# Kernel optimization log

Measured on AMD Instinct MI355X. Metric: run time of the kernel, lower is better.

The kernel has to match this reference:

```python
import jax, jax.numpy as jnp
import numpy as np

N = 100000   # nodes
E = 800000   # edges
D = 128      # hidden_dim (= in_dim here)
H = 4        # heads
C = D // H   # per-head channels = 32
L = 3        # gat layers


def setup_inputs() -> dict:
    key = jax.random.key(0)
    ks = jax.random.split(key, 14)
    s = 0.05
    return {
        "x": jax.random.normal(ks[0], (N, D), dtype=jnp.float32),
        "edge_index": jax.random.randint(ks[1], (2, E), 0, N, dtype=jnp.int32),
        "w_in": jax.random.normal(ks[2], (D, D), dtype=jnp.float32) * s,
        "b_in": jnp.zeros((D,), jnp.float32),
        "Wl": jax.random.normal(ks[3], (L, D, D), dtype=jnp.float32) * s,   # lin_l weights
        "bl": jnp.zeros((L, D), jnp.float32),                               # lin_l bias
        "Wr": jax.random.normal(ks[4], (L, D, D), dtype=jnp.float32) * s,   # lin_r (no bias)
        "att": jax.random.normal(ks[5], (L, H, C), dtype=jnp.float32) * s,  # attention vector a
        "b_out": jnp.zeros((L, D), jnp.float32),                            # conv output bias
        "Wres": jax.random.normal(ks[6], (L - 1, D, D), dtype=jnp.float32) * s,  # residual projs i>0
        "bres": jnp.zeros((L - 1, D), jnp.float32),
        "ln_g": jnp.ones((L, D), jnp.float32),
        "ln_b": jnp.zeros((L, D), jnp.float32),
    }


def _layer_norm(x, g, b, eps=1e-5):
    mu = x.mean(-1, keepdims=True)
    var = ((x - mu) ** 2).mean(-1, keepdims=True)
    return (x - mu) * jax.lax.rsqrt(var + eps) * g + b


def _pairnorm(x, scale=1.0):
    xc = x - x.mean(0, keepdims=True)
    l2 = jnp.sqrt((xc * xc).sum(1, keepdims=True)) + 1e-6
    return xc / l2 * scale * jnp.sqrt(jnp.float32(x.shape[0]))


def _gatv2(x, src, dst, Wl, bl, Wr, att, b_out):
    # lin_l / lin_r projections -> [N, H, C]
    xl = (x @ Wl + bl).reshape(N, H, C)
    xr = (x @ Wr).reshape(N, H, C)
    # edge-wise message: leaky_relu(x_l[j] + x_r[i])  [E, H, C]
    m = jax.nn.leaky_relu(xl[src] + xr[dst], negative_slope=0.2)
    logits = (m * att).sum(-1)  # [E, H]
    # segment softmax over edges grouped by destination node
    lmax = jax.ops.segment_max(logits, dst, num_segments=N)  # [N, H]
    a = jnp.exp(logits - lmax[dst])
    denom = jax.ops.segment_sum(a, dst, num_segments=N)
    a = a / (denom[dst] + 1e-16)
    # aggregate alpha * x_l[j] into destinations, concat heads
    out = jax.ops.segment_sum(a[:, :, None] * xl[src], dst, num_segments=N)
    return out.reshape(N, D) + b_out


def reference(x, edge_index, w_in, b_in, Wl, bl, Wr, att, b_out, Wres, bres, ln_g, ln_b):
    src, dst = edge_index[0], edge_index[1]
    h = x @ w_in + b_in
    for i in range(L):
        identity = h if i == 0 else h @ Wres[i - 1] + bres[i - 1]
        h = _gatv2(h, src, dst, Wl[i], bl[i], Wr[i], att[i], b_out[i])
        h = _pairnorm(h)
        # dropout is identity in eval mode
        h = h + identity
        h = _layer_norm(h, ln_g[i], ln_b[i])
        if i < L - 1:
            h = jax.nn.relu(h)
    return h
```

## Files before the change

### kernel.cpp

```cpp
#include <hip/hip_runtime.h>
#include <hip/hip_bf16.h>

#define NN 100000
#define NE 800000

typedef __attribute__((ext_vector_type(8))) short bf16x8;
typedef __attribute__((ext_vector_type(4))) float f32x4;
typedef unsigned short ushort_t;

static __device__ __forceinline__ short f2bf(float f) {
    union { float f; unsigned u; } v; v.f = f;
    unsigned u = v.u;
    unsigned r = u + 0x7FFFu + ((u >> 16) & 1u);
    return (short)(r >> 16);
}
static __device__ __forceinline__ float bf2f(unsigned short u) {
    union { unsigned u; float f; } v; v.u = ((unsigned)u) << 16;
    return v.f;
}

__global__ void prep_w_k(const float* __restrict__ w_in, const float* __restrict__ Wl,
                         const float* __restrict__ Wr, const float* __restrict__ Wres,
                         ushort_t* __restrict__ wt)
{
    __shared__ float tile[32][33];
    int m = blockIdx.z;
    const float* src;
    if (m == 0)      src = w_in;
    else if (m < 4)  src = Wl + (size_t)(m - 1) * 16384;
    else if (m < 7)  src = Wr + (size_t)(m - 4) * 16384;
    else             src = Wres + (size_t)(m - 7) * 16384;
    ushort_t* dst = wt + (size_t)m * 16384;

    int tx = threadIdx.x, ty = threadIdx.y;
    int k0 = blockIdx.x * 32, c0 = blockIdx.y * 32;
    #pragma unroll
    for (int j = 0; j < 4; ++j)
        tile[ty + 8 * j][tx] = src[(size_t)(k0 + ty + 8 * j) * 128 + c0 + tx];
    __syncthreads();
    #pragma unroll
    for (int j = 0; j < 4; ++j)
        dst[(size_t)(c0 + ty + 8 * j) * 128 + k0 + tx] = (ushort_t)f2bf(tile[tx][ty + 8 * j]);
}

template<int A_FP32>
__global__ __launch_bounds__(256, 4)
void gemm_k(const void* __restrict__ Av, const ushort_t* __restrict__ wt,
            int w0, int w1, int w2,
            const float* __restrict__ bias0, const float* __restrict__ bias2,
            ushort_t* __restrict__ out0, int Dout0, ushort_t* __restrict__ out2, int M)
{
    __shared__ short Bs[128][136];
    const int tid = threadIdx.x;
    const int rowBlk = blockIdx.x * 128;
    const int y = blockIdx.y;
    const ushort_t* W = wt + (size_t)((y == 0) ? w0 : (y == 1) ? w1 : w2) * 16384;
    const float* bias = (y == 0) ? bias0 : ((y == 2) ? bias2 : nullptr);
    ushort_t* out = (y == 2) ? out2 : out0;
    const int Dout   = (y == 2) ? 128 : Dout0;
    const int colOff = (y == 1) ? 128 : 0;

    const int wave = tid >> 6;
    const int lane = tid & 63;
    const int quad = lane >> 4;
    const int lr   = lane & 15;

    const int row0 = rowBlk + wave * 32 + lr;
    const int row1 = row0 + 16;

    bf16x8 afr[4][2];
    #pragma unroll
    for (int ks = 0; ks < 4; ++ks) {
        int kb = ks * 32 + quad * 8;
        bf16x8 a0 = (bf16x8)0, a1 = (bf16x8)0;
        if (A_FP32) {
            const float* A = (const float*)Av;
            if (row0 < M) {
                float4 v0 = *(const float4*)(A + (size_t)row0 * 128 + kb);
                float4 v1 = *(const float4*)(A + (size_t)row0 * 128 + kb + 4);
                a0[0]=f2bf(v0.x); a0[1]=f2bf(v0.y); a0[2]=f2bf(v0.z); a0[3]=f2bf(v0.w);
                a0[4]=f2bf(v1.x); a0[5]=f2bf(v1.y); a0[6]=f2bf(v1.z); a0[7]=f2bf(v1.w);
            }
            if (row1 < M) {
                float4 v0 = *(const float4*)(A + (size_t)row1 * 128 + kb);
                float4 v1 = *(const float4*)(A + (size_t)row1 * 128 + kb + 4);
                a1[0]=f2bf(v0.x); a1[1]=f2bf(v0.y); a1[2]=f2bf(v0.z); a1[3]=f2bf(v0.w);
                a1[4]=f2bf(v1.x); a1[5]=f2bf(v1.y); a1[6]=f2bf(v1.z); a1[7]=f2bf(v1.w);
            }
        } else {
            const ushort_t* A = (const ushort_t*)Av;
            if (row0 < M) a0 = *(const bf16x8*)(A + (size_t)row0 * 128 + kb);
            if (row1 < M) a1 = *(const bf16x8*)(A + (size_t)row1 * 128 + kb);
        }
        afr[ks][0] = a0; afr[ks][1] = a1;
    }

    #pragma unroll
    for (int i = 0; i < 8; ++i) {
        int linear = tid + 256 * i;
        int r  = linear >> 4;
        int c8 = (linear & 15) << 3;
        *(bf16x8*)&Bs[r][c8] = *(const bf16x8*)(W + (size_t)r * 128 + c8);
    }
    __syncthreads();

    f32x4 acc[2][8];
    #pragma unroll
    for (int mt = 0; mt < 2; ++mt)
        #pragma unroll
        for (int nt = 0; nt < 8; ++nt) acc[mt][nt] = (f32x4)(0.0f);

    #pragma unroll
    for (int ks = 0; ks < 4; ++ks) {
        int kb = ks * 32 + quad * 8;
        #pragma unroll
        for (int nt = 0; nt < 8; ++nt) {
            bf16x8 b = *(const bf16x8*)&Bs[nt * 16 + lr][kb];
            acc[0][nt] = __builtin_amdgcn_mfma_f32_16x16x32_bf16(afr[ks][0], b, acc[0][nt], 0, 0, 0);
            acc[1][nt] = __builtin_amdgcn_mfma_f32_16x16x32_bf16(afr[ks][1], b, acc[1][nt], 0, 0, 0);
        }
    }

    __syncthreads();
    #pragma unroll
    for (int mt = 0; mt < 2; ++mt)
        #pragma unroll
        for (int nt = 0; nt < 8; ++nt) {
            int col = nt * 16 + lr;
            float b = bias ? bias[col] : 0.0f;
            #pragma unroll
            for (int r = 0; r < 4; ++r) {
                int row = wave * 32 + mt * 16 + quad * 4 + r;
                Bs[row][col] = f2bf(acc[mt][nt][r] + b);
            }
        }
    __syncthreads();
    #pragma unroll
    for (int i = 0; i < 8; ++i) {
        int linear = tid + 256 * i;
        int r  = linear >> 4;
        int c8 = (linear & 15) << 3;
        int gr = rowBlk + r;
        if (gr < M)
            *(bf16x8*)(out + (size_t)gr * Dout + colOff + c8) = *(const bf16x8*)&Bs[r][c8];
    }
}

__global__ void count_k(const int* __restrict__ dst, int* __restrict__ deg) {
    int e = blockIdx.x * 256 + threadIdx.x;
    if (e < NE) atomicAdd(&deg[dst[e]], 1);
}

__global__ void scan1_k(const int* __restrict__ deg, int* __restrict__ excl,
                        int* __restrict__ bsum) {
    __shared__ int buf[256];
    int i = blockIdx.x * 256 + threadIdx.x;
    int v = (i < NN) ? deg[i] : 0;
    buf[threadIdx.x] = v; __syncthreads();
    for (int off = 1; off < 256; off <<= 1) {
        int t = (threadIdx.x >= off) ? buf[threadIdx.x - off] : 0;
        __syncthreads();
        buf[threadIdx.x] += t;
        __syncthreads();
    }
    if (i < NN) excl[i] = buf[threadIdx.x] - v;
    if (threadIdx.x == 255) bsum[blockIdx.x] = buf[255];
}

__global__ void scan2_k(int* __restrict__ bsum, int nb, int* __restrict__ total) {
    __shared__ int buf[512];
    int v = (threadIdx.x < nb) ? bsum[threadIdx.x] : 0;
    buf[threadIdx.x] = v; __syncthreads();
    for (int off = 1; off < 512; off <<= 1) {
        int t = (threadIdx.x >= off) ? buf[threadIdx.x - off] : 0;
        __syncthreads();
        buf[threadIdx.x] += t;
        __syncthreads();
    }
    if (threadIdx.x < nb) bsum[threadIdx.x] = buf[threadIdx.x] - v;
    if (threadIdx.x == 511) *total = buf[511];
}

__global__ void scan3_k(int* __restrict__ row_ptr, const int* __restrict__ bsum,
                        int* __restrict__ cursor) {
    int i = blockIdx.x * 256 + threadIdx.x;
    if (i < NN) {
        int v = row_ptr[i] + bsum[blockIdx.x];
        row_ptr[i] = v;
        cursor[i]  = v;
    }
}

__global__ void scatter_k(const int* __restrict__ src, const int* __restrict__ dst,
                          int* __restrict__ cursor, int* __restrict__ csr_src) {
    int e = blockIdx.x * 256 + threadIdx.x;
    if (e < NE) {
        int p = atomicAdd(&cursor[dst[e]], 1);
        csr_src[p] = src[e];
    }
}

__global__ __launch_bounds__(256, 8)
void gat_aggregate_k(const ushort_t* __restrict__ xlr, const int* __restrict__ row_ptr,
                     const int* __restrict__ csr_src, const float* __restrict__ att,
                     const float* __restrict__ b_out, ushort_t* __restrict__ g)
{
    int node = blockIdx.x * 4 + (threadIdx.x >> 6);
    int lane = threadIdx.x & 63;
    int slot = lane >> 4;
    int cl   = (lane & 15) << 3;
    bf16x8 xru = *(const bf16x8*)(xlr + (size_t)node * 256 + 128 + cl);
    float xr[8], at4[8];
    #pragma unroll
    for (int j = 0; j < 8; ++j) xr[j] = bf2f((ushort_t)xru[j]);
    float4 at0 = *(const float4*)(att + cl);
    float4 at1 = *(const float4*)(att + cl + 4);
    at4[0] = 0.4f*at0.x; at4[1] = 0.4f*at0.y; at4[2] = 0.4f*at0.z; at4[3] = 0.4f*at0.w;
    at4[4] = 0.4f*at1.x; at4[5] = 0.4f*at1.y; at4[6] = 0.4f*at1.z; at4[7] = 0.4f*at1.w;

    int e0 = row_ptr[node], e1 = row_ptr[node + 1];
    float acc[8] = {0.f,0.f,0.f,0.f,0.f,0.f,0.f,0.f};
    float suma = 0.f;
    for (int e = e0; e < e1; e += 8) {
        int ea = e + slot, eb = e + 4 + slot;
        bool va = ea < e1, vb = eb < e1;
        int sa = csr_src[va ? ea : e];
        int sb = csr_src[vb ? eb : e];
        bf16x8 xua = *(const bf16x8*)(xlr + (size_t)sa * 256 + cl);
        bf16x8 xub = *(const bf16x8*)(xlr + (size_t)sb * 256 + cl);
        float xa[8], xb[8];
        #pragma unroll
        for (int j = 0; j < 8; ++j) { xa[j] = bf2f((ushort_t)xua[j]); xb[j] = bf2f((ushort_t)xub[j]); }
        float pa = 0.f, qa = 0.f, pb = 0.f, qb = 0.f;
        #pragma unroll
        for (int j = 0; j < 8; ++j) {
            float sva = xa[j] + xr[j];
            float svb = xb[j] + xr[j];
            pa = fmaf(at4[j], fabsf(sva), pa);
            qa = fmaf(at4[j], xa[j], qa);
            pb = fmaf(at4[j], fabsf(svb), pb);
            qb = fmaf(at4[j], xb[j], qb);
        }
        float ta = fmaf(1.5f, qa, pa);
        float tb = fmaf(1.5f, qb, pb);
        ta += __shfl_xor(ta, 1); ta += __shfl_xor(ta, 2);
        tb += __shfl_xor(tb, 1); tb += __shfl_xor(tb, 2);
        float aa = va ? __expf(ta) : 0.f;
        float ab = vb ? __expf(tb) : 0.f;
        suma += aa + ab;
        #pragma unroll
        for (int j = 0; j < 8; ++j) acc[j] = fmaf(aa, xa[j], fmaf(ab, xb[j], acc[j]));
    }
    suma += __shfl_xor(suma, 16); suma += __shfl_xor(suma, 32);
    #pragma unroll
    for (int j = 0; j < 8; ++j) {
        acc[j] += __shfl_xor(acc[j], 16);
        acc[j] += __shfl_xor(acc[j], 32);
    }
    if (slot == 0) {
        float inv = 1.0f / (suma + 1e-16f);
        float4 ob0 = *(const float4*)(b_out + cl);
        float4 ob1 = *(const float4*)(b_out + cl + 4);
        float ob[8] = {ob0.x, ob0.y, ob0.z, ob0.w, ob1.x, ob1.y, ob1.z, ob1.w};
        short r[8];
        #pragma unroll
        for (int j = 0; j < 8; ++j) r[j] = f2bf(fmaf(acc[j], inv, ob[j]));
        *(bf16x8*)(g + (size_t)node * 128 + cl) = *(const bf16x8*)r;
    }
}

__global__ void colsum_k(const ushort_t* __restrict__ g, float* __restrict__ colsum) {
    __shared__ float buf[256];
    int c = threadIdx.x & 127;
    int half = threadIdx.x >> 7;
    int r0 = blockIdx.x * 256;
    int rend = min(r0 + 256, NN);
    float s = 0.f;
    for (int r = r0 + half; r < rend; r += 2)
        s += bf2f(g[(size_t)r * 128 + c]);
    buf[threadIdx.x] = s;
    __syncthreads();
    if (threadIdx.x < 128)
        atomicAdd(&colsum[c], buf[threadIdx.x] + buf[threadIdx.x + 128]);
}

__global__ __launch_bounds__(256, 4)
void finalize_k(const ushort_t* __restrict__ g, const float* __restrict__ colsum,
                const ushort_t* __restrict__ ident, const float* __restrict__ lng,
                const float* __restrict__ lnb, ushort_t* __restrict__ hout_bf,
                float* __restrict__ hout_f32, int is_final)
{
    int node = blockIdx.x * 4 + (threadIdx.x >> 6);
    int lane = threadIdx.x & 63;
    int j0 = lane * 2;
    const float invN = 1.0f / (float)NN;
    const float sqrtN = sqrtf((float)NN);

    ushort2 vu = *(const ushort2*)(g + (size_t)node * 128 + j0);
    float x0 = bf2f(vu.x) - colsum[j0] * invN;
    float x1 = bf2f(vu.y) - colsum[j0 + 1] * invN;
    float ss = x0 * x0 + x1 * x1;
    ss += __shfl_xor(ss, 1);  ss += __shfl_xor(ss, 2);  ss += __shfl_xor(ss, 4);
    ss += __shfl_xor(ss, 8);  ss += __shfl_xor(ss, 16); ss += __shfl_xor(ss, 32);
    float sc = sqrtN / (sqrtf(ss) + 1e-6f);

    ushort2 idu = *(const ushort2*)(ident + (size_t)node * 128 + j0);
    float t0 = x0 * sc + bf2f(idu.x);
    float t1 = x1 * sc + bf2f(idu.y);

    float m = t0 + t1;
    m += __shfl_xor(m, 1);  m += __shfl_xor(m, 2);  m += __shfl_xor(m, 4);
    m += __shfl_xor(m, 8);  m += __shfl_xor(m, 16); m += __shfl_xor(m, 32);
    m *= (1.0f / 128.0f);
    float d0 = t0 - m, d1 = t1 - m;
    float vv = d0 * d0 + d1 * d1;
    vv += __shfl_xor(vv, 1);  vv += __shfl_xor(vv, 2);  vv += __shfl_xor(vv, 4);
    vv += __shfl_xor(vv, 8);  vv += __shfl_xor(vv, 16); vv += __shfl_xor(vv, 32);
    vv *= (1.0f / 128.0f);
    float r = rsqrtf(vv + 1e-5f);

    float y0 = d0 * r * lng[j0]     + lnb[j0];
    float y1 = d1 * r * lng[j0 + 1] + lnb[j0 + 1];
    if (is_final) {
        float2 o; o.x = y0; o.y = y1;
        *(float2*)(hout_f32 + (size_t)node * 128 + j0) = o;
    } else {
        y0 = fmaxf(y0, 0.f); y1 = fmaxf(y1, 0.f);
        ushort2 o; o.x = (ushort_t)f2bf(y0); o.y = (ushort_t)f2bf(y1);
        *(ushort2*)(hout_bf + (size_t)node * 128 + j0) = o;
    }
}

extern "C" void kernel_launch(void* const* d_in, const int* in_sizes, int n_in,
                              void* d_out, int out_size, void* d_ws, size_t ws_size,
                              hipStream_t stream) {
    const float* x     = (const float*)d_in[0];
    const int*   ei    = (const int*)  d_in[1];
    const float* w_in  = (const float*)d_in[2];
    const float* b_in  = (const float*)d_in[3];
    const float* Wl    = (const float*)d_in[4];
    const float* bl    = (const float*)d_in[5];
    const float* Wr    = (const float*)d_in[6];
    const float* att   = (const float*)d_in[7];
    const float* b_out = (const float*)d_in[8];
    const float* Wres  = (const float*)d_in[9];
    const float* bres  = (const float*)d_in[10];
    const float* ln_g  = (const float*)d_in[11];
    const float* ln_b  = (const float*)d_in[12];

    ushort_t* h     = (ushort_t*)d_ws;
    ushort_t* xlr   = h + (size_t)NN * 128;
    ushort_t* ident = xlr + (size_t)NN * 256;
    ushort_t* g     = ident + (size_t)NN * 128;
    ushort_t* wt    = g + (size_t)NN * 128;
    int*   row_ptr = (int*)(wt + 9 * 16384);
    int*   cursor  = row_ptr + (NN + 1);
    float* colsum  = (float*)(cursor + NN);
    int*   bsum    = (int*)(colsum + 384);
    int*   csr_src = bsum + 512;

    const int* e_src = ei;
    const int* e_dst = ei + NE;

    hipMemsetAsync(cursor, 0, (size_t)(NN + 384) * 4, stream);

    prep_w_k<<<dim3(4, 4, 9), dim3(32, 8), 0, stream>>>(w_in, Wl, Wr, Wres, wt);

    const int nb = (NN + 255) / 256;
    count_k  <<<NE / 256, 256, 0, stream>>>(e_dst, cursor);
    scan1_k  <<<nb, 256, 0, stream>>>(cursor, row_ptr, bsum);
    scan2_k  <<<1, 512, 0, stream>>>(bsum, nb, row_ptr + NN);
    scan3_k  <<<nb, 256, 0, stream>>>(row_ptr, bsum, cursor);
    scatter_k<<<NE / 256, 256, 0, stream>>>(e_src, e_dst, cursor, csr_src);

    const int gx = (NN + 127) / 128;

    gemm_k<1><<<dim3(gx, 1), 256, 0, stream>>>(x, wt, 0, 0, 0,
                                               b_in, nullptr, h, 128, nullptr, NN);

    for (int i = 0; i < 3; ++i) {
        gemm_k<0><<<dim3(gx, (i > 0) ? 3 : 2), 256, 0, stream>>>(
            h, wt, 1 + i, 4 + i, 7 + (i - 1),
            bl + i * 128, (i > 0) ? (bres + (i - 1) * 128) : nullptr,
            xlr, 256, ident, NN);
        gat_aggregate_k<<<NN / 4, 256, 0, stream>>>(xlr, row_ptr, csr_src,
                                                    att + i * 128, b_out + i * 128, g);
        colsum_k<<<nb, 256, 0, stream>>>(g, colsum + i * 128);
        finalize_k<<<NN / 4, 256, 0, stream>>>(g, colsum + i * 128,
                                               (i == 0) ? h : ident,
                                               ln_g + i * 128, ln_b + i * 128,
                                               h, (float*)d_out, (i == 2) ? 1 : 0);
    }
}
```

Before: 646.9 us.

## Fuse input projection and per-layer GEMMs into one multi-weight kernel

Combines the input projection with layer 0's lin_l/lin_r GEMMs in one kernel. The projected h tile is kept in shared memory and reused as the A operand. Each layer's 2–3 weight GEMMs now run inside a single block that loads A once, instead of using a grid y-dimension that reloads A per weight. This removes one launch and the redundant A reads, but lowers grid parallelism (gx blocks instead of 2–3×gx) and serialises weight loads inside each block.

```diff
diff --git a/kernel.cpp b/kernel.cpp
--- a/kernel.cpp
+++ b/kernel.cpp
@@ -43,38 +43,33 @@
         dst[(size_t)(c0 + ty + 8 * j) * 128 + k0 + tx] = (ushort_t)f2bf(tile[tx][ty + 8 * j]);
 }
 
-template<int A_FP32>
+template<int FUSE_IN>
 __global__ __launch_bounds__(256, 4)
-void gemm_k(const void* __restrict__ Av, const ushort_t* __restrict__ wt,
-            int w0, int w1, int w2,
-            const float* __restrict__ bias0, const float* __restrict__ bias2,
-            ushort_t* __restrict__ out0, int Dout0, ushort_t* __restrict__ out2, int M)
+void gemm_multi_k(const void* __restrict__ Av, const ushort_t* __restrict__ wt,
+                  const float* __restrict__ bfuse, ushort_t* __restrict__ hout,
+                  int w0, int w1, int w2,
+                  const float* __restrict__ bias0, const float* __restrict__ bias2,
+                  ushort_t* __restrict__ out0, ushort_t* __restrict__ out2, int M)
 {
     __shared__ short Bs[128][136];
     const int tid = threadIdx.x;
     const int rowBlk = blockIdx.x * 128;
-    const int y = blockIdx.y;
-    const ushort_t* W = wt + (size_t)((y == 0) ? w0 : (y == 1) ? w1 : w2) * 16384;
-    const float* bias = (y == 0) ? bias0 : ((y == 2) ? bias2 : nullptr);
-    ushort_t* out = (y == 2) ? out2 : out0;
-    const int Dout   = (y == 2) ? 128 : Dout0;
-    const int colOff = (y == 1) ? 128 : 0;
-
     const int wave = tid >> 6;
     const int lane = tid & 63;
     const int quad = lane >> 4;
     const int lr   = lane & 15;
-
     const int row0 = rowBlk + wave * 32 + lr;
     const int row1 = row0 + 16;
 
     bf16x8 afr[4][2];
-    #pragma unroll
-    for (int ks = 0; ks < 4; ++ks) {
-        int kb = ks * 32 + quad * 8;
-        bf16x8 a0 = (bf16x8)0, a1 = (bf16x8)0;
-        if (A_FP32) {
-            const float* A = (const float*)Av;
+    f32x4 acc[2][8];
+
+    if (FUSE_IN) {
+        const float* A = (const float*)Av;
+        #pragma unroll
+        for (int ks = 0; ks < 4; ++ks) {
+            int kb = ks * 32 + quad * 8;
+            bf16x8 a0 = (bf16x8)0, a1 = (bf16x8)0;
             if (row0 < M) {
                 float4 v0 = *(const float4*)(A + (size_t)row0 * 128 + kb);
                 float4 v1 = *(const float4*)(A + (size_t)row0 * 128 + kb + 4);
@@ -87,62 +82,129 @@
                 a1[0]=f2bf(v0.x); a1[1]=f2bf(v0.y); a1[2]=f2bf(v0.z); a1[3]=f2bf(v0.w);
                 a1[4]=f2bf(v1.x); a1[5]=f2bf(v1.y); a1[6]=f2bf(v1.z); a1[7]=f2bf(v1.w);
             }
-        } else {
-            const ushort_t* A = (const ushort_t*)Av;
+            afr[ks][0] = a0; afr[ks][1] = a1;
+        }
+        #pragma unroll
+        for (int i2 = 0; i2 < 8; ++i2) {
+            int linear = tid + 256 * i2;
+            int r  = linear >> 4;
+            int c8 = (linear & 15) << 3;
+            *(bf16x8*)&Bs[r][c8] = *(const bf16x8*)(wt + (size_t)r * 128 + c8);
+        }
+        __syncthreads();
+        #pragma unroll
+        for (int mt = 0; mt < 2; ++mt)
+            #pragma unroll
+            for (int nt = 0; nt < 8; ++nt) acc[mt][nt] = (f32x4)(0.0f);
+        #pragma unroll
+        for (int ks = 0; ks < 4; ++ks) {
+            int kb = ks * 32 + quad * 8;
+            #pragma unroll
+            for (int nt = 0; nt < 8; ++nt) {
+                bf16x8 b = *(const bf16x8*)&Bs[nt * 16 + lr][kb];
+                acc[0][nt] = __builtin_amdgcn_mfma_f32_16x16x32_bf16(afr[ks][0], b, acc[0][nt], 0, 0, 0);
+                acc[1][nt] = __builtin_amdgcn_mfma_f32_16x16x32_bf16(afr[ks][1], b, acc[1][nt], 0, 0, 0);
+            }
+        }
+        __syncthreads();
+        #pragma unroll
+        for (int mt = 0; mt < 2; ++mt)
+            #pragma unroll
+            for (int nt = 0; nt < 8; ++nt) {
+                int col = nt * 16 + lr;
+                float b = bfuse[col];
+                #pragma unroll
+                for (int r = 0; r < 4; ++r) {
+                    int row = wave * 32 + mt * 16 + quad * 4 + r;
+                    Bs[row][col] = f2bf(acc[mt][nt][r] + b);
+                }
+            }
+        __syncthreads();
+        #pragma unroll
+        for (int i2 = 0; i2 < 8; ++i2) {
+            int linear = tid + 256 * i2;
+            int r  = linear >> 4;
+            int c8 = (linear & 15) << 3;
+            int gr = rowBlk + r;
+            if (gr < M)
+                *(bf16x8*)(hout + (size_t)gr * 128 + c8) = *(const bf16x8*)&Bs[r][c8];
+        }
+        #pragma unroll
+        for (int ks = 0; ks < 4; ++ks) {
+            int kb = ks * 32 + quad * 8;
+            afr[ks][0] = *(const bf16x8*)&Bs[wave * 32 + lr][kb];
+            afr[ks][1] = *(const bf16x8*)&Bs[wave * 32 + lr + 16][kb];
+        }
+        __syncthreads();
+    } else {
+        const ushort_t* A = (const ushort_t*)Av;
+        #pragma unroll
+        for (int ks = 0; ks < 4; ++ks) {
+            int kb = ks * 32 + quad * 8;
+            bf16x8 a0 = (bf16x8)0, a1 = (bf16x8)0;
             if (row0 < M) a0 = *(const bf16x8*)(A + (size_t)row0 * 128 + kb);
             if (row1 < M) a1 = *(const bf16x8*)(A + (size_t)row1 * 128 + kb);
-        }
-        afr[ks][0] = a0; afr[ks][1] = a1;
-    }
-
-    #pragma unroll
-    for (int i = 0; i < 8; ++i) {
-        int linear = tid + 256 * i;
-        int r  = linear >> 4;
-        int c8 = (linear & 15) << 3;
-        *(bf16x8*)&Bs[r][c8] = *(const bf16x8*)(W + (size_t)r * 128 + c8);
-    }
-    __syncthreads();
-
-    f32x4 acc[2][8];
-    #pragma unroll
-    for (int mt = 0; mt < 2; ++mt)
-        #pragma unroll
-        for (int nt = 0; nt < 8; ++nt) acc[mt][nt] = (f32x4)(0.0f);
-
-    #pragma unroll
-    for (int ks = 0; ks < 4; ++ks) {
-        int kb = ks * 32 + quad * 8;
-        #pragma unroll
-        for (int nt = 0; nt < 8; ++nt) {
-            bf16x8 b = *(const bf16x8*)&Bs[nt * 16 + lr][kb];
-            acc[0][nt] = __builtin_amdgcn_mfma_f32_16x16x32_bf16(afr[ks][0], b, acc[0][nt], 0, 0, 0);
-            acc[1][nt] = __builtin_amdgcn_mfma_f32_16x16x32_bf16(afr[ks][1], b, acc[1][nt], 0, 0, 0);
-        }
-    }
-
-    __syncthreads();
-    #pragma unroll
-    for (int mt = 0; mt < 2; ++mt)
-        #pragma unroll
-        for (int nt = 0; nt < 8; ++nt) {
-            int col = nt * 16 + lr;
-            float b = bias ? bias[col] : 0.0f;
-            #pragma unroll
-            for (int r = 0; r < 4; ++r) {
-                int row = wave * 32 + mt * 16 + quad * 4 + r;
-                Bs[row][col] = f2bf(acc[mt][nt][r] + b);
-            }
-        }
-    __syncthreads();
-    #pragma unroll
-    for (int i = 0; i < 8; ++i) {
-        int linear = tid + 256 * i;
-        int r  = linear >> 4;
-        int c8 = (linear & 15) << 3;
-        int gr = rowBlk + r;
-        if (gr < M)
-            *(bf16x8*)(out + (size_t)gr * Dout + colOff + c8) = *(const bf16x8*)&Bs[r][c8];
+            afr[ks][0] = a0; afr[ks][1] = a1;
+        }
+    }
+
+    for (int t = 0; t < 3; ++t) {
+        int widx = (t == 0) ? w0 : (t == 1) ? w1 : w2;
+        if (widx < 0) break;
+        const ushort_t* W = wt + (size_t)widx * 16384;
+        const float* bias = (t == 0) ? bias0 : ((t == 2) ? bias2 : nullptr);
+        ushort_t* dst   = (t == 2) ? out2 : out0;
+        const int Dout  = (t == 2) ? 128 : 256;
+        const int colOff = (t == 1) ? 128 : 0;
+
+        if (t > 0) __syncthreads();
+        #pragma unroll
+        for (int i2 = 0; i2 < 8; ++i2) {
+            int linear = tid + 256 * i2;
+            int r  = linear >> 4;
+            int c8 = (linear & 15) << 3;
+            *(bf16x8*)&Bs[r][c8] = *(const bf16x8*)(W + (size_t)r * 128 + c8);
+        }
+        __syncthreads();
+
+        #pragma unroll
+        for (int mt = 0; mt < 2; ++mt)
+            #pragma unroll
+            for (int nt = 0; nt < 8; ++nt) acc[mt][nt] = (f32x4)(0.0f);
+        #pragma unroll
+        for (int ks = 0; ks < 4; ++ks) {
+            int kb = ks * 32 + quad * 8;
+            #pragma unroll
+            for (int nt = 0; nt < 8; ++nt) {
+                bf16x8 b = *(const bf16x8*)&Bs[nt * 16 + lr][kb];
+                acc[0][nt] = __builtin_amdgcn_mfma_f32_16x16x32_bf16(afr[ks][0], b, acc[0][nt], 0, 0, 0);
+                acc[1][nt] = __builtin_amdgcn_mfma_f32_16x16x32_bf16(afr[ks][1], b, acc[1][nt], 0, 0, 0);
+            }
+        }
+        __syncthreads();
+
+        #pragma unroll
+        for (int mt = 0; mt < 2; ++mt)
+            #pragma unroll
+            for (int nt = 0; nt < 8; ++nt) {
+                int col = nt * 16 + lr;
+                float b = bias ? bias[col] : 0.0f;
+                #pragma unroll
+                for (int r = 0; r < 4; ++r) {
+                    int row = wave * 32 + mt * 16 + quad * 4 + r;
+                    Bs[row][col] = f2bf(acc[mt][nt][r] + b);
+                }
+            }
+        __syncthreads();
+        #pragma unroll
+        for (int i2 = 0; i2 < 8; ++i2) {
+            int linear = tid + 256 * i2;
+            int r  = linear >> 4;
+            int c8 = (linear & 15) << 3;
+            int gr = rowBlk + r;
+            if (gr < M)
+                *(bf16x8*)(dst + (size_t)gr * Dout + colOff + c8) = *(const bf16x8*)&Bs[r][c8];
+        }
     }
 }
 
@@ -375,14 +437,15 @@
 
     const int gx = (NN + 127) / 128;
 
-    gemm_k<1><<<dim3(gx, 1), 256, 0, stream>>>(x, wt, 0, 0, 0,
-                                               b_in, nullptr, h, 128, nullptr, NN);
-
     for (int i = 0; i < 3; ++i) {
-        gemm_k<0><<<dim3(gx, (i > 0) ? 3 : 2), 256, 0, stream>>>(
-            h, wt, 1 + i, 4 + i, 7 + (i - 1),
-            bl + i * 128, (i > 0) ? (bres + (i - 1) * 128) : nullptr,
-            xlr, 256, ident, NN);
+        if (i == 0)
+            gemm_multi_k<1><<<gx, 256, 0, stream>>>(
+                x, wt, b_in, h, 1, 4, -1,
+                bl, nullptr, xlr, nullptr, NN);
+        else
+            gemm_multi_k<0><<<gx, 256, 0, stream>>>(
+                h, wt, nullptr, nullptr, 1 + i, 4 + i, 7 + (i - 1),
+                bl + i * 128, bres + (i - 1) * 128, xlr, ident, NN);
         gat_aggregate_k<<<NN / 4, 256, 0, stream>>>(xlr, row_ptr, csr_src,
                                                     att + i * 128, b_out + i * 128, g);
         colsum_k<<<nb, 256, 0, stream>>>(g, colsum + i * 128);
```

Measured after the change: 703.1 us. 8.7% more time.

## Prefetch CSR indices in GAT aggregate and vectorize colsum/finalize kernels

Applied to the files above, without the earlier changes.

In the aggregation loop, the source indices for the next group of 8 edges are now loaded one iteration ahead, so the dependent index-then-gather load chain overlaps with current work. The column-sum and finalize kernels are rewritten to use 16-byte bf16x8 loads, with 16 lanes per node instead of 64. Finalize processes 16 nodes per block and needs fewer shuffle steps. Occupancy hints are raised to 8. The prefetch reads one extra index per iteration (clamped to e0) and adds some register pressure.

```diff
diff --git a/kernel.cpp b/kernel.cpp
--- a/kernel.cpp
+++ b/kernel.cpp
@@ -221,13 +221,22 @@
     int e0 = row_ptr[node], e1 = row_ptr[node + 1];
     float acc[8] = {0.f,0.f,0.f,0.f,0.f,0.f,0.f,0.f};
     float suma = 0.f;
+
+    int sa = 0, sb = 0;
+    if (e0 < e1) {
+        int ea = e0 + slot, eb = e0 + 4 + slot;
+        sa = csr_src[ea < e1 ? ea : e0];
+        sb = csr_src[eb < e1 ? eb : e0];
+    }
     for (int e = e0; e < e1; e += 8) {
-        int ea = e + slot, eb = e + 4 + slot;
-        bool va = ea < e1, vb = eb < e1;
-        int sa = csr_src[va ? ea : e];
-        int sb = csr_src[vb ? eb : e];
+        bool va = (e + slot) < e1, vb = (e + 4 + slot) < e1;
         bf16x8 xua = *(const bf16x8*)(xlr + (size_t)sa * 256 + cl);
         bf16x8 xub = *(const bf16x8*)(xlr + (size_t)sb * 256 + cl);
+        {
+            int ea2 = e + 8 + slot, eb2 = e + 12 + slot;
+            sa = csr_src[ea2 < e1 ? ea2 : e0];
+            sb = csr_src[eb2 < e1 ? eb2 : e0];
+        }
         float xa[8], xb[8];
         #pragma unroll
         for (int j = 0; j < 8; ++j) { xa[j] = bf2f((ushort_t)xua[j]); xb[j] = bf2f((ushort_t)xub[j]); }
@@ -269,65 +278,102 @@
     }
 }
 
-__global__ void colsum_k(const ushort_t* __restrict__ g, float* __restrict__ colsum) {
-    __shared__ float buf[256];
-    int c = threadIdx.x & 127;
-    int half = threadIdx.x >> 7;
+__global__ __launch_bounds__(256, 8)
+void colsum_k(const ushort_t* __restrict__ g, float* __restrict__ colsum) {
+    __shared__ float buf[16][128];
+    int c8 = (threadIdx.x & 15) << 3;
+    int rg = threadIdx.x >> 4;
     int r0 = blockIdx.x * 256;
-    int rend = min(r0 + 256, NN);
-    float s = 0.f;
-    for (int r = r0 + half; r < rend; r += 2)
-        s += bf2f(g[(size_t)r * 128 + c]);
-    buf[threadIdx.x] = s;
+    float s[8] = {0.f,0.f,0.f,0.f,0.f,0.f,0.f,0.f};
+    #pragma unroll 4
+    for (int it = 0; it < 16; ++it) {
+        int r = r0 + rg + (it << 4);
+        if (r < NN) {
+            bf16x8 v = *(const bf16x8*)(g + (size_t)r * 128 + c8);
+            #pragma unroll
+            for (int j = 0; j < 8; ++j) s[j] += bf2f((ushort_t)v[j]);
+        }
+    }
+    #pragma unroll
+    for (int j = 0; j < 8; ++j) buf[rg][c8 + j] = s[j];
     __syncthreads();
-    if (threadIdx.x < 128)
-        atomicAdd(&colsum[c], buf[threadIdx.x] + buf[threadIdx.x + 128]);
-}
-
-__global__ __launch_bounds__(256, 4)
+    if (threadIdx.x < 128) {
+        float t = 0.f;
+        #pragma unroll
+        for (int k = 0; k < 16; ++k) t += buf[k][threadIdx.x];
+        atomicAdd(&colsum[threadIdx.x], t);
+    }
+}
+
+__global__ __launch_bounds__(256, 8)
 void finalize_k(const ushort_t* __restrict__ g, const float* __restrict__ colsum,
                 const ushort_t* __restrict__ ident, const float* __restrict__ lng,
                 const float* __restrict__ lnb, ushort_t* __restrict__ hout_bf,
                 float* __restrict__ hout_f32, int is_final)
 {
-    int node = blockIdx.x * 4 + (threadIdx.x >> 6);
     int lane = threadIdx.x & 63;
-    int j0 = lane * 2;
+    int li   = lane & 15;
+    int node = blockIdx.x * 16 + ((threadIdx.x >> 6) << 2) + (lane >> 4);
+    int c8   = li << 3;
     const float invN = 1.0f / (float)NN;
     const float sqrtN = sqrtf((float)NN);
 
-    ushort2 vu = *(const ushort2*)(g + (size_t)node * 128 + j0);
-    float x0 = bf2f(vu.x) - colsum[j0] * invN;
-    float x1 = bf2f(vu.y) - colsum[j0 + 1] * invN;
-    float ss = x0 * x0 + x1 * x1;
-    ss += __shfl_xor(ss, 1);  ss += __shfl_xor(ss, 2);  ss += __shfl_xor(ss, 4);
-    ss += __shfl_xor(ss, 8);  ss += __shfl_xor(ss, 16); ss += __shfl_xor(ss, 32);
+    bf16x8 vu = *(const bf16x8*)(g + (size_t)node * 128 + c8);
+    float4 cs0 = *(const float4*)(colsum + c8);
+    float4 cs1 = *(const float4*)(colsum + c8 + 4);
+    float cs[8] = {cs0.x, cs0.y, cs0.z, cs0.w, cs1.x, cs1.y, cs1.z, cs1.w};
+    float x[8], ss = 0.f;
+    #pragma unroll
+    for (int j = 0; j < 8; ++j) {
+        x[j] = bf2f((ushort_t)vu[j]) - cs[j] * invN;
+        ss = fmaf(x[j], x[j], ss);
+    }
+    ss += __shfl_xor(ss, 1); ss += __shfl_xor(ss, 2);
+    ss += __shfl_xor(ss, 4); ss += __shfl_xor(ss, 8);
     float sc = sqrtN / (sqrtf(ss) + 1e-6f);
 
-    ushort2 idu = *(const ushort2*)(ident + (size_t)node * 128 + j0);
-    float t0 = x0 * sc + bf2f(idu.x);
-    float t1 = x1 * sc + bf2f(idu.y);
-
-    float m = t0 + t1;
-    m += __shfl_xor(m, 1);  m += __shfl_xor(m, 2);  m += __shfl_xor(m, 4);
-    m += __shfl_xor(m, 8);  m += __shfl_xor(m, 16); m += __shfl_xor(m, 32);
+    bf16x8 idu = *(const bf16x8*)(ident + (size_t)node * 128 + c8);
+    float t[8], m = 0.f;
+    #pragma unroll
+    for (int j = 0; j < 8; ++j) {
+        t[j] = fmaf(x[j], sc, bf2f((ushort_t)idu[j]));
+        m += t[j];
+    }
+    m += __shfl_xor(m, 1); m += __shfl_xor(m, 2);
+    m += __shfl_xor(m, 4); m += __shfl_xor(m, 8);
     m *= (1.0f / 128.0f);
-    float d0 = t0 - m, d1 = t1 - m;
-    float vv = d0 * d0 + d1 * d1;
-    vv += __shfl_xor(vv, 1);  vv += __shfl_xor(vv, 2);  vv += __shfl_xor(vv, 4);
-    vv += __shfl_xor(vv, 8);  vv += __shfl_xor(vv, 16); vv += __shfl_xor(vv, 32);
+    float d[8], vv = 0.f;
+    #pragma unroll
+    for (int j = 0; j < 8; ++j) { d[j] = t[j] - m; vv = fmaf(d[j], d[j], vv); }
+    vv += __shfl_xor(vv, 1); vv += __shfl_xor(vv, 2);
+    vv += __shfl_xor(vv, 4); vv += __shfl_xor(vv, 8);
     vv *= (1.0f / 128.0f);
     float r = rsqrtf(vv + 1e-5f);
 
-    float y0 = d0 * r * lng[j0]     + lnb[j0];
-    float y1 = d1 * r * lng[j0 + 1] + lnb[j0 + 1];
+    float4 lg0 = *(const float4*)(lng + c8);
+    float4 lg1 = *(const float4*)(lng + c8 + 4);
+    float4 lb0 = *(const float4*)(lnb + c8);
+    float4 lb1 = *(const float4*)(lnb + c8 + 4);
+    float lg[8] = {lg0.x, lg0.y, lg0.z, lg0.w, lg1.x, lg1.y, lg1.z, lg1.w};
+    float lb[8] = {lb0.x, lb0.y, lb0.z, lb0.w, lb1.x, lb1.y, lb1.z, lb1.w};
+
     if (is_final) {
-        float2 o; o.x = y0; o.y = y1;
-        *(float2*)(hout_f32 + (size_t)node * 128 + j0) = o;
+        float y[8];
+        #pragma unroll
+        for (int j = 0; j < 8; ++j) y[j] = fmaf(d[j] * r, lg[j], lb[j]);
+        float* op = hout_f32 + (size_t)node * 128 + c8;
+        float4 o0, o1;
+        o0.x=y[0]; o0.y=y[1]; o0.z=y[2]; o0.w=y[3];
+        o1.x=y[4]; o1.y=y[5]; o1.z=y[6]; o1.w=y[7];
+        *(float4*)op = o0; *(float4*)(op + 4) = o1;
     } else {
-        y0 = fmaxf(y0, 0.f); y1 = fmaxf(y1, 0.f);
-        ushort2 o; o.x = (ushort_t)f2bf(y0); o.y = (ushort_t)f2bf(y1);
-        *(ushort2*)(hout_bf + (size_t)node * 128 + j0) = o;
+        short o[8];
+        #pragma unroll
+        for (int j = 0; j < 8; ++j) {
+            float y = fmaf(d[j] * r, lg[j], lb[j]);
+            o[j] = f2bf(fmaxf(y, 0.f));
+        }
+        *(bf16x8*)(hout_bf + (size_t)node * 128 + c8) = *(const bf16x8*)o;
     }
 }
 
@@ -386,9 +432,9 @@
         gat_aggregate_k<<<NN / 4, 256, 0, stream>>>(xlr, row_ptr, csr_src,
                                                     att + i * 128, b_out + i * 128, g);
         colsum_k<<<nb, 256, 0, stream>>>(g, colsum + i * 128);
-        finalize_k<<<NN / 4, 256, 0, stream>>>(g, colsum + i * 128,
-                                               (i == 0) ? h : ident,
-                                               ln_g + i * 128, ln_b + i * 128,
-                                               h, (float*)d_out, (i == 2) ? 1 : 0);
-    }
-}
+        finalize_k<<<NN / 16, 256, 0, stream>>>(g, colsum + i * 128,
+                                                (i == 0) ? h : ident,
+                                                ln_g + i * 128, ln_b + i * 128,
+                                                h, (float*)d_out, (i == 2) ? 1 : 0);
+    }
+}
```

Result: faster. 560.9 us (-13.3%).
